# Kernel optimization log

Hardware: AMD Instinct MI355X
Metric: run time of the kernel (lower is better)

## Reference

```python
import jax, jax.numpy as jnp
import numpy as np

N1, N2, F = 2048, 32768, 64
SPATIAL = 512  # fine (big) spatial size
I = 3          # 2**I * coarse_size = SPATIAL


def setup_inputs() -> dict:
    key = jax.random.key(0)
    k1, k2, k3 = jax.random.split(key, 3)
    coarse_size = SPATIAL // (2 ** I)  # 64
    # coarse voxel coords: 3 spatial dims in [0, coarse_size), batch col = 0
    fm_sp = jax.random.randint(k1, (N1, 3), 0, coarse_size)
    feature_map = jnp.concatenate([fm_sp, jnp.zeros((N1, 1), jnp.int32)], axis=1).astype(jnp.float32)
    # fine voxel coords: 3 spatial dims in [0, SPATIAL), batch col = 0
    co_sp = jax.random.randint(k2, (N2, 3), 0, SPATIAL)
    coords = jnp.concatenate([co_sp, jnp.zeros((N2, 1), jnp.int32)], axis=1).astype(jnp.float32)
    x_features = jax.random.normal(k3, (N1, F), dtype=jnp.float32)
    return {"feature_map": feature_map, "x_features": x_features, "coords": coords, "i": I}


def reference(feature_map, x_features, coords, i):
    scale = 2 ** i
    # (N1,1,4) vs (1,N2,4) broadcast containment test (all 4 columns, incl. batch id,
    # are scaled — faithful to the original module)
    fm_scaled = feature_map * scale                      # (N1,4)
    lo = fm_scaled[:, None, :] <= coords[None, :, :]     # (N1,N2,4)
    hi = (fm_scaled[:, None, :] + scale) > coords[None, :, :]
    index = lo.all(-1) & hi.all(-1)                      # (N1,N2) bool
    # torch.t(index).argmax(dim=1): for each fine voxel, first coarse voxel containing it
    sel = jnp.argmax(index, axis=0)                      # (N2,)
    final_features = x_features[sel]                     # (N2,F)
    final_coords = feature_map[sel]                      # (N2,4)
    return final_coords, final_features
```

## Files before the change

kernel.cpp:

```cpp
#include <hip/hip_runtime.h>

#define N1 2048
#define N2 32768
#define F  64
#define SPATIAL 512
#define EMPTY 0x7fffffff

__global__ void efm_init_grid(int* __restrict__ grid, int n) {
    int idx = blockIdx.x * blockDim.x + threadIdx.x;
    if (idx < n) grid[idx] = EMPTY;
}

__global__ void efm_populate(const float* __restrict__ fm,
                             const int* __restrict__ ip,
                             int* __restrict__ grid) {
    int n1 = blockIdx.x * blockDim.x + threadIdx.x;
    if (n1 >= N1) return;
    int i  = ip[0];
    int cs = SPATIAL >> i;
    float4 f = ((const float4*)fm)[n1];
    int x = (int)f.x, y = (int)f.y, z = (int)f.z;
    atomicMin(&grid[(x * cs + y) * cs + z], n1);
}

__global__ void efm_gather(const float* __restrict__ fm,
                           const float* __restrict__ xf,
                           const float* __restrict__ co,
                           const int*   __restrict__ ip,
                           const int*   __restrict__ grid,
                           float* __restrict__ out_coords,
                           float* __restrict__ out_feats) {
    int tid  = blockIdx.x * blockDim.x + threadIdx.x;
    int n2   = tid >> 6;
    int lane = tid & 63;
    if (n2 >= N2) return;
    int i  = ip[0];
    int cs = SPATIAL >> i;
    float4 c = ((const float4*)co)[n2];
    int cx = ((int)c.x) >> i;
    int cy = ((int)c.y) >> i;
    int cz = ((int)c.z) >> i;
    int sel = grid[(cx * cs + cy) * cs + cz];
    if (sel == EMPTY) sel = 0;
    out_feats[n2 * F + lane] = xf[sel * F + lane];
    if (lane < 4) out_coords[n2 * 4 + lane] = fm[sel * 4 + lane];
}

__global__ void efm_brute(const float* __restrict__ fm,
                          const float* __restrict__ xf,
                          const float* __restrict__ co,
                          const int*   __restrict__ ip,
                          float* __restrict__ out_coords,
                          float* __restrict__ out_feats) {
    int tid  = blockIdx.x * blockDim.x + threadIdx.x;
    int n2   = tid >> 6;
    int lane = tid & 63;
    if (n2 >= N2) return;
    float scale = (float)(1 << ip[0]);
    float4 c = ((const float4*)co)[n2];
    int sel = 0;
    for (int base = 0; base < N1; base += 64) {
        float4 f = ((const float4*)fm)[base + lane];
        bool m = (f.x * scale <= c.x) && (f.x * scale + scale > c.x)
              && (f.y * scale <= c.y) && (f.y * scale + scale > c.y)
              && (f.z * scale <= c.z) && (f.z * scale + scale > c.z)
              && (f.w * scale <= c.w) && (f.w * scale + scale > c.w);
        unsigned long long b = __ballot(m);
        if (b) { sel = base + __ffsll((unsigned long long)b) - 1; break; }
    }
    out_feats[n2 * F + lane] = xf[sel * F + lane];
    if (lane < 4) out_coords[n2 * 4 + lane] = fm[sel * 4 + lane];
}

extern "C" void kernel_launch(void* const* d_in, const int* in_sizes, int n_in,
                              void* d_out, int out_size, void* d_ws, size_t ws_size,
                              hipStream_t stream) {
    const float* fm = (const float*)d_in[0];
    const float* xf = (const float*)d_in[1];
    const float* co = (const float*)d_in[2];
    const int*   ip = (const int*)d_in[3];

    float* out_coords = (float*)d_out;
    float* out_feats  = (float*)d_out + N2 * 4;

    const size_t grid_cells = 64 * 64 * 64;
    if (ws_size >= grid_cells * sizeof(int)) {
        int* grid = (int*)d_ws;
        efm_init_grid<<<(int)((grid_cells + 255) / 256), 256, 0, stream>>>(
            grid, (int)grid_cells);
        efm_populate<<<(N1 + 255) / 256, 256, 0, stream>>>(fm, ip, grid);
        efm_gather<<<(N2 * 64 + 255) / 256, 256, 0, stream>>>(
            fm, xf, co, ip, grid, out_coords, out_feats);
    } else {
        efm_brute<<<(N2 * 64 + 255) / 256, 256, 0, stream>>>(
            fm, xf, co, ip, out_coords, out_feats);
    }
}
```

Baseline: 70.90 us.

## Fuse grid build and gather into one kernel with shared-memory cell scan

Replaces the three-kernel path (grid init, atomic populate, gather) with a single kernel. Each block packs all coarse voxel coordinates into integer cell ids in shared memory, then eight threads per fine voxel scan them for the first match and reduce with shuffles before gathering features. This drops two extra launches and the 1 MB grid initialization, at the cost of every block redundantly rebuilding and scanning 2048 cells. The packed id assumes coordinates fit in 6 bits, which depends on i=3.

```diff
diff --git a/kernel.cpp b/kernel.cpp
--- a/kernel.cpp
+++ b/kernel.cpp
@@ -1,75 +1,74 @@
 #include <hip/hip_runtime.h>
 
-#define N1 2048
-#define N2 32768
-#define F  64
-#define SPATIAL 512
-#define EMPTY 0x7fffffff
 
-__global__ void efm_init_grid(int* __restrict__ grid, int n) {
-    int idx = blockIdx.x * blockDim.x + threadIdx.x;
-    if (idx < n) grid[idx] = EMPTY;
-}
+#define N1    2048
+#define N2    32768
+#define F     64
+#define VPB   32
+#define TPV   8
+#define BLOCK 256
+#define NBLOCKS (N2 / VPB)
 
-__global__ void efm_populate(const float* __restrict__ fm,
-                             const int* __restrict__ ip,
-                             int* __restrict__ grid) {
-    int n1 = blockIdx.x * blockDim.x + threadIdx.x;
-    if (n1 >= N1) return;
-    int i  = ip[0];
-    int cs = SPATIAL >> i;
-    float4 f = ((const float4*)fm)[n1];
-    int x = (int)f.x, y = (int)f.y, z = (int)f.z;
-    atomicMin(&grid[(x * cs + y) * cs + z], n1);
-}
+__global__ __launch_bounds__(BLOCK)
+void efm_fused(const float* __restrict__ fm,
+               const float* __restrict__ xf,
+               const float* __restrict__ co,
+               const int*   __restrict__ ip,
+               float* __restrict__ out_coords,
+               float* __restrict__ out_feats) {
+    __shared__ int cells[N1];
+    __shared__ int selArr[VPB];
 
-__global__ void efm_gather(const float* __restrict__ fm,
-                           const float* __restrict__ xf,
-                           const float* __restrict__ co,
-                           const int*   __restrict__ ip,
-                           const int*   __restrict__ grid,
-                           float* __restrict__ out_coords,
-                           float* __restrict__ out_feats) {
-    int tid  = blockIdx.x * blockDim.x + threadIdx.x;
-    int n2   = tid >> 6;
-    int lane = tid & 63;
-    if (n2 >= N2) return;
-    int i  = ip[0];
-    int cs = SPATIAL >> i;
-    float4 c = ((const float4*)co)[n2];
-    int cx = ((int)c.x) >> i;
-    int cy = ((int)c.y) >> i;
-    int cz = ((int)c.z) >> i;
-    int sel = grid[(cx * cs + cy) * cs + cz];
-    if (sel == EMPTY) sel = 0;
-    out_feats[n2 * F + lane] = xf[sel * F + lane];
-    if (lane < 4) out_coords[n2 * 4 + lane] = fm[sel * 4 + lane];
-}
+    const int t = threadIdx.x;
+    const int i = ip[0];
 
-__global__ void efm_brute(const float* __restrict__ fm,
-                          const float* __restrict__ xf,
-                          const float* __restrict__ co,
-                          const int*   __restrict__ ip,
-                          float* __restrict__ out_coords,
-                          float* __restrict__ out_feats) {
-    int tid  = blockIdx.x * blockDim.x + threadIdx.x;
-    int n2   = tid >> 6;
-    int lane = tid & 63;
-    if (n2 >= N2) return;
-    float scale = (float)(1 << ip[0]);
-    float4 c = ((const float4*)co)[n2];
-    int sel = 0;
-    for (int base = 0; base < N1; base += 64) {
-        float4 f = ((const float4*)fm)[base + lane];
-        bool m = (f.x * scale <= c.x) && (f.x * scale + scale > c.x)
-              && (f.y * scale <= c.y) && (f.y * scale + scale > c.y)
-              && (f.z * scale <= c.z) && (f.z * scale + scale > c.z)
-              && (f.w * scale <= c.w) && (f.w * scale + scale > c.w);
-        unsigned long long b = __ballot(m);
-        if (b) { sel = base + __ffsll((unsigned long long)b) - 1; break; }
+    #pragma unroll
+    for (int r = t; r < N1; r += BLOCK) {
+        float4 f = ((const float4*)fm)[r];
+        int id = ((((((int)f.w << 6) | (int)f.x) << 6) | (int)f.y) << 6) | (int)f.z;
+        cells[r] = id;
     }
-    out_feats[n2 * F + lane] = xf[sel * F + lane];
-    if (lane < 4) out_coords[n2 * 4 + lane] = fm[sel * 4 + lane];
+    __syncthreads();
+
+    const int vox  = t >> 3;
+    const int sub  = t & 7;
+    const int gvox = blockIdx.x * VPB + vox;
+
+    float4 c = ((const float4*)co)[gvox];
+    int cid = (((((((int)c.w >> i) << 6) | ((int)c.x >> i)) << 6)
+                 | ((int)c.y >> i)) << 6) | ((int)c.z >> i);
+
+    int local = N1;
+    const int4* cells4 = (const int4*)cells;
+    #pragma unroll 4
+    for (int k = 0; k < N1 / (4 * TPV); ++k) {
+        int idx4 = k * TPV + sub;
+        int4 v = cells4[idx4];
+        int j = idx4 * 4;
+        if (v.x == cid) local = min(local, j);
+        if (v.y == cid) local = min(local, j + 1);
+        if (v.z == cid) local = min(local, j + 2);
+        if (v.w == cid) local = min(local, j + 3);
+    }
+    local = min(local, __shfl_down(local, 4, 8));
+    local = min(local, __shfl_down(local, 2, 8));
+    local = min(local, __shfl_down(local, 1, 8));
+    if (sub == 0) selArr[vox] = (local < N1) ? local : 0;
+    __syncthreads();
+
+    const int lane = t & 63;
+    const int wv   = t >> 6;
+    #pragma unroll
+    for (int v = 0; v < 8; ++v) {
+        int lv  = wv * 8 + v;
+        int sel = selArr[lv];
+        out_feats[(size_t)(blockIdx.x * VPB + lv) * F + lane] = xf[sel * F + lane];
+    }
+    if (t < VPB * 4) {
+        int lv = t >> 2, comp = t & 3;
+        int sel = selArr[lv];
+        out_coords[(blockIdx.x * VPB + lv) * 4 + comp] = fm[sel * 4 + comp];
+    }
 }
 
 extern "C" void kernel_launch(void* const* d_in, const int* in_sizes, int n_in,
@@ -83,16 +82,5 @@
     float* out_coords = (float*)d_out;
     float* out_feats  = (float*)d_out + N2 * 4;
 
-    const size_t grid_cells = 64 * 64 * 64;
-    if (ws_size >= grid_cells * sizeof(int)) {
-        int* grid = (int*)d_ws;
-        efm_init_grid<<<(int)((grid_cells + 255) / 256), 256, 0, stream>>>(
-            grid, (int)grid_cells);
-        efm_populate<<<(N1 + 255) / 256, 256, 0, stream>>>(fm, ip, grid);
-        efm_gather<<<(N2 * 64 + 255) / 256, 256, 0, stream>>>(
-            fm, xf, co, ip, grid, out_coords, out_feats);
-    } else {
-        efm_brute<<<(N2 * 64 + 255) / 256, 256, 0, stream>>>(
-            fm, xf, co, ip, out_coords, out_feats);
-    }
+    efm_fused<<<NBLOCKS, BLOCK, 0, stream>>>(fm, xf, co, ip, out_coords, out_feats);
 }
```

Measured after the change: 71.72 us. Within noise of the previous version (+1.2%).
